# Optimization experiments

Measured on AMD Instinct MI355X. Metric: run time of the kernel, lower is better.

## Reference

```python
import jax, jax.numpy as jnp
import numpy as np

B, L, D_MODEL, N_HEADS = 2, 2048, 1024, 16
HEAD_DIM = D_MODEL // N_HEADS  # 64
PAD_START = (3 * L) // 4  # last quarter of keys are padding


def _rope_tables(seq_len, dim, base=10000.0, dtype=jnp.float32):
    inv_freq = 1.0 / (base ** (jnp.arange(0, dim, 2, dtype=jnp.float32) / dim))
    t = jnp.arange(seq_len, dtype=jnp.float32)
    freqs = jnp.einsum('i,j->ij', t, inv_freq)  # (L, dim/2)
    return jnp.cos(freqs).astype(dtype), jnp.sin(freqs).astype(dtype)


def _apply_rope(x, cos, sin):
    # x: (B, H, L, D); cos/sin: (L, D/2)
    cos = cos[None, None]
    sin = sin[None, None]
    x_even, x_odd = x[..., 0::2], x[..., 1::2]
    rot_even = x_even * cos - x_odd * sin
    rot_odd = x_even * sin + x_odd * cos
    return jnp.stack((rot_even, rot_odd), axis=-1).reshape(x.shape)


def setup_inputs() -> dict:
    key = jax.random.key(0)
    k_x, k_wqkv, k_bqkv, k_wout, k_bout = jax.random.split(key, 5)
    x = jax.random.normal(k_x, (B, L, D_MODEL), dtype=jnp.float32)
    Wqkv = jax.random.normal(k_wqkv, (3 * D_MODEL, D_MODEL), dtype=jnp.float32) * 0.02
    bqkv = jax.random.normal(k_bqkv, (3 * D_MODEL,), dtype=jnp.float32) * 0.02
    Wout = jax.random.normal(k_wout, (D_MODEL, D_MODEL), dtype=jnp.float32) * 0.02
    bout = jax.random.normal(k_bout, (D_MODEL,), dtype=jnp.float32) * 0.02
    # True = padded position (end of sequence padded)
    pad_mask = jnp.broadcast_to(jnp.arange(L) >= PAD_START, (B, L))
    return {"x": x, "pad_mask": pad_mask, "Wqkv": Wqkv, "bqkv": bqkv, "Wout": Wout, "bout": bout}


def reference(x, pad_mask, Wqkv, bqkv, Wout, bout):
    Bc, Lc, E = x.shape
    H, D = N_HEADS, HEAD_DIM
    qkv = x @ Wqkv.T + bqkv                       # (B, L, 3E)
    qkv = qkv.reshape(Bc, Lc, 3, H, D)
    q = jnp.transpose(qkv[:, :, 0], (0, 2, 1, 3))  # (B, H, L, D)
    k = jnp.transpose(qkv[:, :, 1], (0, 2, 1, 3))
    v = jnp.transpose(qkv[:, :, 2], (0, 2, 1, 3))
    cos, sin = _rope_tables(Lc, D, dtype=x.dtype)
    q = _apply_rope(q, cos, sin)
    k = _apply_rope(k, cos, sin)
    # Mask exactly as the torch module builds it: attn_mask = causal_upper | key_pad,
    # with torch bool-mask semantics (True = allowed to attend).
    causal_upper = jnp.triu(jnp.ones((Lc, Lc), dtype=bool), 1)[None, None]  # (1,1,L,L)
    key_pad = pad_mask[:, None, None, :]                                     # (B,1,1,L)
    allowed = causal_upper | key_pad                                         # (B,1,L,L)
    scale = 1.0 / jnp.sqrt(jnp.asarray(D, dtype=x.dtype))
    scores = jnp.einsum('bhqd,bhkd->bhqk', q, k) * scale
    scores = jnp.where(allowed, scores, -jnp.inf)
    attn = jax.nn.softmax(scores, axis=-1)
    out = jnp.einsum('bhqk,bhkd->bhqd', attn, v)   # (B, H, L, D)
    out = jnp.transpose(out, (0, 2, 1, 3)).reshape(Bc, Lc, E)
    return out @ Wout.T + bout
```

## Files before the change

### kernel.cpp

```cpp
#include <hip/hip_runtime.h>

#define BB 2
#define LL 2048
#define DM 1024
#define NH 16
#define HD 64
#define PAD_START 1536

typedef short bf16x8 __attribute__((ext_vector_type(8)));
typedef float f32x4 __attribute__((ext_vector_type(4)));

#define MFMA_B16(a, b, c) __builtin_amdgcn_mfma_f32_16x16x32_bf16(a, b, c, 0, 0, 0)

#define GLOAD_LDS16(g, l)                                            \
    __builtin_amdgcn_global_load_lds(                                \
        (const __attribute__((address_space(1))) void*)(g),          \
        (__attribute__((address_space(3))) void*)(l), 16, 0, 0)

__device__ __forceinline__ float bf2f(unsigned short u) {
    union { unsigned int i; float f; } v; v.i = ((unsigned int)u) << 16; return v.f;
}
__device__ __forceinline__ unsigned short f2bf(float f) {
    union { float f; unsigned int i; } v; v.f = f;
    unsigned int x = v.i;
    return (unsigned short)((x + 0x7fffu + ((x >> 16) & 1u)) >> 16);
}

__global__ __launch_bounds__(256) void split_kernel(
    const float* __restrict__ X, const float* __restrict__ Wq,
    const float* __restrict__ Wo,
    unsigned short* __restrict__ Xh,
    unsigned short* __restrict__ Wh,
    unsigned short* __restrict__ Woh,
    float* __restrict__ cosT, float* __restrict__ sinT)
{
    if (blockIdx.x >= 8192) {
        const int idx = (blockIdx.x - 8192) * 256 + threadIdx.x;
        const int l = idx >> 5, pp = idx & 31;
        const float LOG2_1E4 = 13.287712379549449f;
        const float invf = exp2f(-((float)pp) * (LOG2_1E4 / 32.0f));
        const float ang = (float)l * invf;
        cosT[idx] = cosf(ang);
        sinT[idx] = sinf(ang);
        return;
    }
    const size_t e = ((size_t)blockIdx.x * 256 + threadIdx.x) * 4;
    const float* src; unsigned short* dh; size_t o;
    if (e < 4194304)      { src = X;  dh = Xh;  o = e; }
    else if (e < 7340032) { src = Wq; dh = Wh;  o = e - 4194304; }
    else                  { src = Wo; dh = Woh; o = e - 7340032; }
    float4 v = *(const float4*)(src + o);
    ushort4 hv;
    hv.x = f2bf(v.x); hv.y = f2bf(v.y);
    hv.z = f2bf(v.z); hv.w = f2bf(v.w);
    *(ushort4*)(dh + o) = hv;
}

#define ACC_PARAMS f32x4& c00, f32x4& c01, f32x4& c02, f32x4& c03, \
                   f32x4& c10, f32x4& c11, f32x4& c12, f32x4& c13, \
                   f32x4& c20, f32x4& c21, f32x4& c22, f32x4& c23, \
                   f32x4& c30, f32x4& c31, f32x4& c32, f32x4& c33
#define ACC_ARGS c00, c01, c02, c03, c10, c11, c12, c13, \
                 c20, c21, c22, c23, c30, c31, c32, c33

__device__ __forceinline__ void gemm_bk64(
    const unsigned short* __restrict__ A, const unsigned short* __restrict__ B,
    int m0, int n0, unsigned short* As, unsigned short* Bs, ACC_PARAMS)
{
    const int t = threadIdx.x;
    const int lane = t & 63;
    const int w = t >> 6;
    const int wm = (w >> 1) << 6;
    const int wn = (w & 1) << 6;
    const int lm = lane & 15;
    const int quad = lane >> 4;

    const int rop = lane >> 3;
    const int sw  = ((lane & 7) ^ rop) * 8;
    const unsigned short* ga = A + (size_t)(m0 + w * 32 + rop) * 1024 + sw;
    const unsigned short* gb = B + (size_t)(n0 + w * 32 + rop) * 1024 + sw;
    unsigned short* lA = As + (w * 32) * 64;
    unsigned short* lB = Bs + (w * 32) * 64;

    const int o1 = (quad ^ (lm & 7)) * 8;
    const int o2 = ((quad + 4) ^ (lm & 7)) * 8;
    const int arow = (wm + lm) * 64;
    const int brow = (wn + lm) * 64;

    for (int k0 = 0; k0 < 1024; k0 += 64) {
        __syncthreads();
        GLOAD_LDS16(ga + k0,             lA);
        GLOAD_LDS16(ga + k0 +  8 * 1024, lA +  8 * 64);
        GLOAD_LDS16(ga + k0 + 16 * 1024, lA + 16 * 64);
        GLOAD_LDS16(ga + k0 + 24 * 1024, lA + 24 * 64);
        GLOAD_LDS16(gb + k0,             lB);
        GLOAD_LDS16(gb + k0 +  8 * 1024, lB +  8 * 64);
        GLOAD_LDS16(gb + k0 + 16 * 1024, lB + 16 * 64);
        GLOAD_LDS16(gb + k0 + 24 * 1024, lB + 24 * 64);
        __syncthreads();
        {
            bf16x8 a0 = *(const bf16x8*)(As + arow +  0 * 64 + o1);
            bf16x8 a1 = *(const bf16x8*)(As + arow + 16 * 64 + o1);
            bf16x8 a2 = *(const bf16x8*)(As + arow + 32 * 64 + o1);
            bf16x8 a3 = *(const bf16x8*)(As + arow + 48 * 64 + o1);
            bf16x8 b0 = *(const bf16x8*)(Bs + brow +  0 * 64 + o1);
            bf16x8 b1 = *(const bf16x8*)(Bs + brow + 16 * 64 + o1);
            bf16x8 b2 = *(const bf16x8*)(Bs + brow + 32 * 64 + o1);
            bf16x8 b3 = *(const bf16x8*)(Bs + brow + 48 * 64 + o1);
            c00 = MFMA_B16(a0, b0, c00); c01 = MFMA_B16(a0, b1, c01);
            c02 = MFMA_B16(a0, b2, c02); c03 = MFMA_B16(a0, b3, c03);
            c10 = MFMA_B16(a1, b0, c10); c11 = MFMA_B16(a1, b1, c11);
            c12 = MFMA_B16(a1, b2, c12); c13 = MFMA_B16(a1, b3, c13);
            c20 = MFMA_B16(a2, b0, c20); c21 = MFMA_B16(a2, b1, c21);
            c22 = MFMA_B16(a2, b2, c22); c23 = MFMA_B16(a2, b3, c23);
            c30 = MFMA_B16(a3, b0, c30); c31 = MFMA_B16(a3, b1, c31);
            c32 = MFMA_B16(a3, b2, c32); c33 = MFMA_B16(a3, b3, c33);
        }
        {
            bf16x8 a0 = *(const bf16x8*)(As + arow +  0 * 64 + o2);
            bf16x8 a1 = *(const bf16x8*)(As + arow + 16 * 64 + o2);
            bf16x8 a2 = *(const bf16x8*)(As + arow + 32 * 64 + o2);
            bf16x8 a3 = *(const bf16x8*)(As + arow + 48 * 64 + o2);
            bf16x8 b0 = *(const bf16x8*)(Bs + brow +  0 * 64 + o2);
            bf16x8 b1 = *(const bf16x8*)(Bs + brow + 16 * 64 + o2);
            bf16x8 b2 = *(const bf16x8*)(Bs + brow + 32 * 64 + o2);
            bf16x8 b3 = *(const bf16x8*)(Bs + brow + 48 * 64 + o2);
            c00 = MFMA_B16(a0, b0, c00); c01 = MFMA_B16(a0, b1, c01);
            c02 = MFMA_B16(a0, b2, c02); c03 = MFMA_B16(a0, b3, c03);
            c10 = MFMA_B16(a1, b0, c10); c11 = MFMA_B16(a1, b1, c11);
            c12 = MFMA_B16(a1, b2, c12); c13 = MFMA_B16(a1, b3, c13);
            c20 = MFMA_B16(a2, b0, c20); c21 = MFMA_B16(a2, b1, c21);
            c22 = MFMA_B16(a2, b2, c22); c23 = MFMA_B16(a2, b3, c23);
            c30 = MFMA_B16(a3, b0, c30); c31 = MFMA_B16(a3, b1, c31);
            c32 = MFMA_B16(a3, b2, c32); c33 = MFMA_B16(a3, b3, c33);
        }
    }
}

__device__ __forceinline__ void qk_frag(
    f32x4 cf, int r0, int bh, int d, float bv, float qscale,
    const float* __restrict__ cosT, const float* __restrict__ sinT,
    unsigned short* __restrict__ dst, bool odd)
{
    const int p = d >> 1;
#pragma unroll
    for (int e = 0; e < 4; ++e) {
        const int l = (r0 + e) & (LL - 1);
        const float x = cf[e] + bv;
        const float px = __shfl_xor(x, 1);
        const float cs = cosT[l * 32 + p];
        const float sn = sinT[l * 32 + p];
        const float ve = odd ? px : x;
        const float vo = odd ? x : px;
        float res = odd ? (ve * sn + vo * cs) : (ve * cs - vo * sn);
        res *= qscale;
        const float other = __shfl_xor(res, 1);
        if (!odd) {
            const unsigned int pk = ((unsigned int)f2bf(res)) |
                                    (((unsigned int)f2bf(other)) << 16);
            *(unsigned int*)(dst + ((size_t)bh * LL + l) * HD + d) = pk;
        }
    }
}

__device__ __forceinline__ void v_frag(
    f32x4 cf, int l0, int bh, int d, float bv, unsigned short* __restrict__ vt)
{
    ushort4 pk;
    pk.x = f2bf(cf[0] + bv); pk.y = f2bf(cf[1] + bv);
    pk.z = f2bf(cf[2] + bv); pk.w = f2bf(cf[3] + bv);
    *(ushort4*)(vt + ((size_t)(bh * HD + d)) * LL + l0) = pk;
}

__device__ __forceinline__ void out_frag(
    f32x4 cf, int r0, int c, float bv, float* __restrict__ C)
{
#pragma unroll
    for (int e = 0; e < 4; ++e)
        C[(size_t)(r0 + e) * DM + c] = cf[e] + bv;
}

__global__ __launch_bounds__(256) void qkv_mfma(
    const unsigned short* __restrict__ Xh,
    const unsigned short* __restrict__ Wh,
    const float* __restrict__ bias,
    const float* __restrict__ cosT, const float* __restrict__ sinT,
    unsigned short* __restrict__ qs, unsigned short* __restrict__ ks,
    unsigned short* __restrict__ vt)
{
    __shared__ unsigned short As[128 * 64];
    __shared__ unsigned short Bs[128 * 64];
    const int n0 = blockIdx.x * 128;
    const int m0 = blockIdx.y * 128;
    f32x4 c00 = {0,0,0,0}, c01 = {0,0,0,0}, c02 = {0,0,0,0}, c03 = {0,0,0,0};
    f32x4 c10 = {0,0,0,0}, c11 = {0,0,0,0}, c12 = {0,0,0,0}, c13 = {0,0,0,0};
    f32x4 c20 = {0,0,0,0}, c21 = {0,0,0,0}, c22 = {0,0,0,0}, c23 = {0,0,0,0};
    f32x4 c30 = {0,0,0,0}, c31 = {0,0,0,0}, c32 = {0,0,0,0}, c33 = {0,0,0,0};

    gemm_bk64(Xh, Wh, m0, n0, As, Bs, ACC_ARGS);

    const int t = threadIdx.x;
    const int lane = t & 63;
    const int w = t >> 6;
    const int wm = (w >> 1) << 6;
    const int wn = (w & 1) << 6;
    const int lm = lane & 15;
    const int quad = lane >> 4;

    const int s = n0 >> 10;
    const int cb = n0 + wn;
    const int h = (cb >> 6) & (NH - 1);
    const int bi = m0 >> 11;
    const int bh = bi * NH + h;
    const int rbase = m0 + wm;

    if (s == 2) {
#define VSTORE(rt, ct) \
        v_frag(c##rt##ct, (rbase + rt * 16 + quad * 4) & (LL - 1), bh, \
               ct * 16 + lm, bias[cb + ct * 16 + lm], vt);
        VSTORE(0,0) VSTORE(0,1) VSTORE(0,2) VSTORE(0,3)
        VSTORE(1,0) VSTORE(1,1) VSTORE(1,2) VSTORE(1,3)
        VSTORE(2,0) VSTORE(2,1) VSTORE(2,2) VSTORE(2,3)
        VSTORE(3,0) VSTORE(3,1) VSTORE(3,2) VSTORE(3,3)
#undef VSTORE
    } else {
        unsigned short* dst = (s == 0) ? qs : ks;
        const float qscale = (s == 0) ? 0.125f : 1.0f;
        const bool odd = (lm & 1) != 0;
#define QKSTORE(rt, ct) \
        qk_frag(c##rt##ct, rbase + rt * 16 + quad * 4, bh, ct * 16 + lm, \
                bias[cb + ct * 16 + lm], qscale, cosT, sinT, dst, odd);
        QKSTORE(0,0) QKSTORE(0,1) QKSTORE(0,2) QKSTORE(0,3)
        QKSTORE(1,0) QKSTORE(1,1) QKSTORE(1,2) QKSTORE(1,3)
        QKSTORE(2,0) QKSTORE(2,1) QKSTORE(2,2) QKSTORE(2,3)
        QKSTORE(3,0) QKSTORE(3,1) QKSTORE(3,2) QKSTORE(3,3)
#undef QKSTORE
    }
}

__global__ __launch_bounds__(256) void attn_mfma(
    const unsigned short* __restrict__ qs,
    const unsigned short* __restrict__ ks,
    const unsigned short* __restrict__ vt,
    unsigned short* __restrict__ aoh)
{
    __shared__ unsigned short Ks[64 * 72];
    __shared__ unsigned short Vs[64 * 72];
    __shared__ unsigned short Pl[4][16 * 72];

    const int bh = blockIdx.y;
    const int qt = (blockIdx.x + blockIdx.y) & 31;
    const int q0 = qt * 64;
    const int b = bh >> 4, h = bh & (NH - 1);
    const int tid = threadIdx.x;
    const int w = tid >> 6;
    const int lane = tid & 63;
    const int lm = lane & 15;
    const int quad = lane >> 4;
    const int qw0 = q0 + w * 16;

    const unsigned short* qbase = qs + ((size_t)bh * LL + qw0 + lm) * HD + quad * 8;
    const bf16x8 qf0 = *(const bf16x8*)(qbase);
    const bf16x8 qf1 = *(const bf16x8*)(qbase + 32);

    f32x4 O[4];
#pragma unroll
    for (int dd = 0; dd < 4; ++dd) O[dd] = (f32x4){0.f, 0.f, 0.f, 0.f};
    float lrow[4] = {0.f, 0.f, 0.f, 0.f};

    const unsigned short* kbase = ks + (size_t)bh * LL * HD;
    const unsigned short* vtb   = vt + (size_t)bh * HD * LL;
    unsigned short* pw = &Pl[w][0];

    const int srow = tid >> 3;
    const int sch  = (tid & 7) * 8;

    const int t0 = ((q0 < PAD_START) ? q0 : PAD_START) >> 6;

    int k0 = t0 * 64;
    uint4 ka0 = *(const uint4*)(kbase + (size_t)(k0 + srow) * HD + sch);
    uint4 ka1 = *(const uint4*)(kbase + (size_t)(k0 + srow + 32) * HD + sch);
    uint4 va0 = *(const uint4*)(vtb + (size_t)srow * LL + k0 + sch);
    uint4 va1 = *(const uint4*)(vtb + (size_t)(srow + 32) * LL + k0 + sch);

    for (int tt = t0; tt < 32; ++tt) {
        k0 = tt * 64;
        __syncthreads();
        *(uint4*)(Ks + srow * 72 + sch)        = ka0;
        *(uint4*)(Ks + (srow + 32) * 72 + sch) = ka1;
        *(uint4*)(Vs + srow * 72 + sch)        = va0;
        *(uint4*)(Vs + (srow + 32) * 72 + sch) = va1;
        __syncthreads();

        {
            const int kn = ((tt + 1) < 32 ? (tt + 1) : 31) * 64;
            ka0 = *(const uint4*)(kbase + (size_t)(kn + srow) * HD + sch);
            ka1 = *(const uint4*)(kbase + (size_t)(kn + srow + 32) * HD + sch);
            va0 = *(const uint4*)(vtb + (size_t)srow * LL + kn + sch);
            va1 = *(const uint4*)(vtb + (size_t)(srow + 32) * LL + kn + sch);
        }

        f32x4 sfrag[4];
#pragma unroll
        for (int c = 0; c < 4; ++c) {
            const bf16x8 kf0 = *(const bf16x8*)(Ks + (c * 16 + lm) * 72 + quad * 8);
            const bf16x8 kf1 = *(const bf16x8*)(Ks + (c * 16 + lm) * 72 + 32 + quad * 8);
            f32x4 z = (f32x4){0.f, 0.f, 0.f, 0.f};
            z = MFMA_B16(qf0, kf0, z);
            z = MFMA_B16(qf1, kf1, z);
            sfrag[c] = z;
        }
        if (tt == t0 && q0 < PAD_START) {
#pragma unroll
            for (int c = 0; c < 4; ++c) {
                const int kg = k0 + c * 16 + lm;
#pragma unroll
                for (int r = 0; r < 4; ++r) {
                    const int qg = qw0 + quad * 4 + r;
                    if (kg <= qg) sfrag[c][r] = -1e30f;
                }
            }
        }
#pragma unroll
        for (int r = 0; r < 4; ++r) {
#pragma unroll
            for (int c = 0; c < 4; ++c) {
                const float p = __expf(sfrag[c][r]);
                lrow[r] += p;
                pw[(quad * 4 + r) * 72 + c * 16 + lm] = f2bf(p);
            }
        }
        const bf16x8 a0 = *(const bf16x8*)(pw + lm * 72 + quad * 8);
        const bf16x8 a1 = *(const bf16x8*)(pw + lm * 72 + 32 + quad * 8);
#pragma unroll
        for (int dd = 0; dd < 4; ++dd) {
            const bf16x8 b0 = *(const bf16x8*)(Vs + (dd * 16 + lm) * 72 + quad * 8);
            const bf16x8 b1 = *(const bf16x8*)(Vs + (dd * 16 + lm) * 72 + 32 + quad * 8);
            O[dd] = MFMA_B16(a0, b0, O[dd]);
            O[dd] = MFMA_B16(a1, b1, O[dd]);
        }
    }

#pragma unroll
    for (int r = 0; r < 4; ++r) {
        float rs = lrow[r];
        rs += __shfl_xor(rs, 1);
        rs += __shfl_xor(rs, 2);
        rs += __shfl_xor(rs, 4);
        rs += __shfl_xor(rs, 8);
        lrow[r] = rs;
    }

#pragma unroll
    for (int r = 0; r < 4; ++r) {
        const float inv = 1.0f / lrow[r];
        const int qg = qw0 + quad * 4 + r;
        const size_t base = ((size_t)(b * LL + qg)) * DM + h * HD;
#pragma unroll
        for (int dd = 0; dd < 4; ++dd)
            aoh[base + dd * 16 + lm] = f2bf(O[dd][r] * inv);
    }
}

__global__ __launch_bounds__(256) void out_mfma(
    const unsigned short* __restrict__ Ah,
    const unsigned short* __restrict__ Wh,
    const float* __restrict__ bias, float* __restrict__ C)
{
    __shared__ unsigned short As[128 * 64];
    __shared__ unsigned short Bs[128 * 64];
    const int n0 = blockIdx.x * 128;
    const int m0 = blockIdx.y * 128;

    f32x4 c00 = {0,0,0,0}, c01 = {0,0,0,0}, c02 = {0,0,0,0}, c03 = {0,0,0,0};
    f32x4 c10 = {0,0,0,0}, c11 = {0,0,0,0}, c12 = {0,0,0,0}, c13 = {0,0,0,0};
    f32x4 c20 = {0,0,0,0}, c21 = {0,0,0,0}, c22 = {0,0,0,0}, c23 = {0,0,0,0};
    f32x4 c30 = {0,0,0,0}, c31 = {0,0,0,0}, c32 = {0,0,0,0}, c33 = {0,0,0,0};

    gemm_bk64(Ah, Wh, m0, n0, As, Bs, ACC_ARGS);

    const int t = threadIdx.x;
    const int lane = t & 63;
    const int w = t >> 6;
    const int wm = (w >> 1) << 6;
    const int wn = (w & 1) << 6;
    const int lm = lane & 15;
    const int quad = lane >> 4;

#define CSTORE(rt, ct) \
    out_frag(c##rt##ct, m0 + wm + rt * 16 + quad * 4, \
             n0 + wn + ct * 16 + lm, bias[n0 + wn + ct * 16 + lm], C);
    CSTORE(0,0) CSTORE(0,1) CSTORE(0,2) CSTORE(0,3)
    CSTORE(1,0) CSTORE(1,1) CSTORE(1,2) CSTORE(1,3)
    CSTORE(2,0) CSTORE(2,1) CSTORE(2,2) CSTORE(2,3)
    CSTORE(3,0) CSTORE(3,1) CSTORE(3,2) CSTORE(3,3)
#undef CSTORE
}

extern "C" void kernel_launch(void* const* d_in, const int* in_sizes, int n_in,
                              void* d_out, int out_size, void* d_ws, size_t ws_size,
                              hipStream_t stream)
{
    const float* x    = (const float*)d_in[0];
    const float* Wqkv = (const float*)d_in[2];
    const float* bqkv = (const float*)d_in[3];
    const float* Wout = (const float*)d_in[4];
    const float* bout = (const float*)d_in[5];
    float* out = (float*)d_out;

    unsigned short* p = (unsigned short*)d_ws;
    const size_t SZ = (size_t)BB * NH * LL * HD;
    unsigned short* qsb = p; p += SZ;
    unsigned short* ksb = p; p += SZ;
    unsigned short* vtb = p; p += SZ;
    unsigned short* Xhi = p; p += SZ;
    unsigned short* Whi = p; p += (size_t)3145728;
    unsigned short* Wohi = p; p += (size_t)1048576;
    float* cosT = (float*)p; p += (size_t)2 * 65536;
    float* sinT = (float*)p; p += (size_t)2 * 65536;

    split_kernel<<<8448, 256, 0, stream>>>(x, Wqkv, Wout,
                                           Xhi, Whi, Wohi, cosT, sinT);
    dim3 g1(24, 32);
    qkv_mfma<<<g1, 256, 0, stream>>>(Xhi, Whi, bqkv, cosT, sinT,
                                     qsb, ksb, vtb);
    dim3 g2(32, 32);
    attn_mfma<<<g2, 256, 0, stream>>>(qsb, ksb, vtb, Xhi);
    dim3 g3(8, 32);
    out_mfma<<<g3, 256, 0, stream>>>(Xhi, Wohi, bout, out);
}
```

Before: 223.1 us.

## Double-buffer K/V tiles in LDS with XOR-swizzled layout in attention kernel

Converts the attention kernel's K/V shared-memory staging to a two-buffer ping-pong, so each iteration writes the next tile while computing on the current one. This cuts the loop from two barriers to one. It also replaces the padded 72-stride rows with 64-stride rows addressed through an XOR swizzle, for K, V and the per-warp P scratch, to avoid LDS bank conflicts. LDS use per block rises for the second K/V buffer, which may affect occupancy.

```diff
diff --git a/kernel.cpp b/kernel.cpp
--- a/kernel.cpp
+++ b/kernel.cpp
@@ -244,9 +244,9 @@
     const unsigned short* __restrict__ vt,
     unsigned short* __restrict__ aoh)
 {
-    __shared__ unsigned short Ks[64 * 72];
-    __shared__ unsigned short Vs[64 * 72];
-    __shared__ unsigned short Pl[4][16 * 72];
+    __shared__ unsigned short Ks[2][64 * 64];
+    __shared__ unsigned short Vs[2][64 * 64];
+    __shared__ unsigned short Pl[4][16 * 64];
 
     const int bh = blockIdx.y;
     const int qt = (blockIdx.x + blockIdx.y) & 31;
@@ -274,37 +274,58 @@
 
     const int srow = tid >> 3;
     const int sch  = (tid & 7) * 8;
+    const int ps   = (((tid & 7) ^ (srow & 7)) * 8);
+
+    const int o1 = (quad ^ (lm & 7)) * 8;
+    const int o2 = ((quad + 4) ^ (lm & 7)) * 8;
 
     const int t0 = ((q0 < PAD_START) ? q0 : PAD_START) >> 6;
 
-    int k0 = t0 * 64;
-    uint4 ka0 = *(const uint4*)(kbase + (size_t)(k0 + srow) * HD + sch);
-    uint4 ka1 = *(const uint4*)(kbase + (size_t)(k0 + srow + 32) * HD + sch);
-    uint4 va0 = *(const uint4*)(vtb + (size_t)srow * LL + k0 + sch);
-    uint4 va1 = *(const uint4*)(vtb + (size_t)(srow + 32) * LL + k0 + sch);
+    int kc = t0 * 64;
+    uint4 ka0 = *(const uint4*)(kbase + (size_t)(kc + srow) * HD + sch);
+    uint4 ka1 = *(const uint4*)(kbase + (size_t)(kc + srow + 32) * HD + sch);
+    uint4 va0 = *(const uint4*)(vtb + (size_t)srow * LL + kc + sch);
+    uint4 va1 = *(const uint4*)(vtb + (size_t)(srow + 32) * LL + kc + sch);
+    *(uint4*)(&Ks[0][srow * 64 + ps])        = ka0;
+    *(uint4*)(&Ks[0][(srow + 32) * 64 + ps]) = ka1;
+    *(uint4*)(&Vs[0][srow * 64 + ps])        = va0;
+    *(uint4*)(&Vs[0][(srow + 32) * 64 + ps]) = va1;
+    if (t0 + 1 < 32) {
+        const int kn = (t0 + 1) * 64;
+        ka0 = *(const uint4*)(kbase + (size_t)(kn + srow) * HD + sch);
+        ka1 = *(const uint4*)(kbase + (size_t)(kn + srow + 32) * HD + sch);
+        va0 = *(const uint4*)(vtb + (size_t)srow * LL + kn + sch);
+        va1 = *(const uint4*)(vtb + (size_t)(srow + 32) * LL + kn + sch);
+    }
+    __syncthreads();
 
     for (int tt = t0; tt < 32; ++tt) {
-        k0 = tt * 64;
-        __syncthreads();
-        *(uint4*)(Ks + srow * 72 + sch)        = ka0;
-        *(uint4*)(Ks + (srow + 32) * 72 + sch) = ka1;
-        *(uint4*)(Vs + srow * 72 + sch)        = va0;
-        *(uint4*)(Vs + (srow + 32) * 72 + sch) = va1;
-        __syncthreads();
-
-        {
-            const int kn = ((tt + 1) < 32 ? (tt + 1) : 31) * 64;
+        const int s = (tt - t0) & 1;
+        const unsigned short* Kc = &Ks[s][0];
+        const unsigned short* Vc = &Vs[s][0];
+        unsigned short* Ko = &Ks[s ^ 1][0];
+        unsigned short* Vo = &Vs[s ^ 1][0];
+
+        if (tt + 1 < 32) {
+            *(uint4*)(Ko + srow * 64 + ps)        = ka0;
+            *(uint4*)(Ko + (srow + 32) * 64 + ps) = ka1;
+            *(uint4*)(Vo + srow * 64 + ps)        = va0;
+            *(uint4*)(Vo + (srow + 32) * 64 + ps) = va1;
+        }
+        if (tt + 2 < 32) {
+            const int kn = (tt + 2) * 64;
             ka0 = *(const uint4*)(kbase + (size_t)(kn + srow) * HD + sch);
             ka1 = *(const uint4*)(kbase + (size_t)(kn + srow + 32) * HD + sch);
             va0 = *(const uint4*)(vtb + (size_t)srow * LL + kn + sch);
             va1 = *(const uint4*)(vtb + (size_t)(srow + 32) * LL + kn + sch);
         }
 
+        const int k0 = tt * 64;
         f32x4 sfrag[4];
 #pragma unroll
         for (int c = 0; c < 4; ++c) {
-            const bf16x8 kf0 = *(const bf16x8*)(Ks + (c * 16 + lm) * 72 + quad * 8);
-            const bf16x8 kf1 = *(const bf16x8*)(Ks + (c * 16 + lm) * 72 + 32 + quad * 8);
+            const bf16x8 kf0 = *(const bf16x8*)(Kc + (c * 16 + lm) * 64 + o1);
+            const bf16x8 kf1 = *(const bf16x8*)(Kc + (c * 16 + lm) * 64 + o2);
             f32x4 z = (f32x4){0.f, 0.f, 0.f, 0.f};
             z = MFMA_B16(qf0, kf0, z);
             z = MFMA_B16(qf1, kf1, z);
@@ -323,22 +344,26 @@
         }
 #pragma unroll
         for (int r = 0; r < 4; ++r) {
+            const int prow = quad * 4 + r;
+            const int pbase = prow * 64 + (lm & 7);
+            const int pr7 = prow & 7;
 #pragma unroll
             for (int c = 0; c < 4; ++c) {
                 const float p = __expf(sfrag[c][r]);
                 lrow[r] += p;
-                pw[(quad * 4 + r) * 72 + c * 16 + lm] = f2bf(p);
+                pw[pbase + (((c * 2 + (lm >> 3)) ^ pr7) * 8)] = f2bf(p);
             }
         }
-        const bf16x8 a0 = *(const bf16x8*)(pw + lm * 72 + quad * 8);
-        const bf16x8 a1 = *(const bf16x8*)(pw + lm * 72 + 32 + quad * 8);
+        const bf16x8 a0 = *(const bf16x8*)(pw + lm * 64 + o1);
+        const bf16x8 a1 = *(const bf16x8*)(pw + lm * 64 + o2);
 #pragma unroll
         for (int dd = 0; dd < 4; ++dd) {
-            const bf16x8 b0 = *(const bf16x8*)(Vs + (dd * 16 + lm) * 72 + quad * 8);
-            const bf16x8 b1 = *(const bf16x8*)(Vs + (dd * 16 + lm) * 72 + 32 + quad * 8);
+            const bf16x8 b0 = *(const bf16x8*)(Vc + (dd * 16 + lm) * 64 + o1);
+            const bf16x8 b1 = *(const bf16x8*)(Vc + (dd * 16 + lm) * 64 + o2);
             O[dd] = MFMA_B16(a0, b0, O[dd]);
             O[dd] = MFMA_B16(a1, b1, O[dd]);
         }
+        __syncthreads();
     }
 
 #pragma unroll
```

Result: slower. 228.3 us (+2.4%).
